# Kernel tuning notes

Measured on AMD Instinct MI355X. Metric: run time of the kernel, lower is better.

Reference implementation:

```python
import jax, jax.numpy as jnp
import numpy as np
from jax import lax

D = 1024
T = 1024
B = 8


def setup_inputs() -> dict:
    key = jax.random.key(0)
    ks = jax.random.split(key, 4)
    x = jax.random.normal(ks[0], (T, B, D), dtype=jnp.float32)
    h0 = jnp.zeros((B, D), dtype=jnp.float32)
    # xavier-ish scale for input projections, small orthogonal-like scale for W_h
    xav = float(np.sqrt(2.0 / (D + D)))
    W_alpha = jax.random.normal(ks[1], (D, D), dtype=jnp.float32) * xav
    b_alpha = jnp.full((D,), 2.0, dtype=jnp.float32)  # init_alpha_bias=2.0
    W_h = jax.random.normal(ks[2], (D, D), dtype=jnp.float32) * (0.5 / np.sqrt(D))
    W_x = jax.random.normal(ks[3], (D, D), dtype=jnp.float32) * xav
    b = jnp.zeros((D,), dtype=jnp.float32)
    return {"x": x, "h0": h0, "W_alpha": W_alpha, "b_alpha": b_alpha,
            "W_h": W_h, "W_x": W_x, "b": b}


def reference(x, h0, W_alpha, b_alpha, W_h, W_x, b):
    # x: [T,B,D], h0: [B,D]; E63a nonlinear delta recurrence.
    # Precompute input-dependent parts (parallel over T), scan the recurrence.
    alpha_all = jax.nn.sigmoid(jnp.einsum('tbd,ed->tbe', x, W_alpha) + b_alpha)  # [T,B,D]
    wx_all = jnp.einsum('tbd,ed->tbe', x, W_x) + b                               # [T,B,D]

    def step(h_prev, inp):
        alpha, wx = inp
        v = jnp.tanh(h_prev @ W_h.T + wx)          # nonlinear value in h
        h_new = alpha * h_prev + (1.0 - alpha) * v  # complementary gate
        out = h_new * jax.nn.silu(h_new)            # gated output
        return h_new, (h_new, out)

    _, (hs, outs) = lax.scan(step, h0, (alpha_all, wx_all))
    h = jnp.concatenate([h0[None], hs], axis=0)  # [T+1,B,D] (matches torch path)
    return outs, h
```

## Files before the change

kernel.cpp:

```cpp
#include <hip/hip_runtime.h>
#include <hip/hip_bf16.h>
#include <hip/hip_cooperative_groups.h>

typedef __attribute__((ext_vector_type(8))) short bf16x8;
typedef __attribute__((ext_vector_type(4))) float f32x4;
typedef __attribute__((ext_vector_type(4))) unsigned int u32x4;

#define D_ 1024
#define T_ 1024
#define B_ 8
#define M_ (T_ * B_)

__device__ __forceinline__ float ldv(const float* p) { return *p; }
__device__ __forceinline__ float ldv(const __hip_bfloat16* p) { return __bfloat162float(*p); }
__device__ __forceinline__ void stv(float* p, float v) { *p = v; }
__device__ __forceinline__ void stv(__hip_bfloat16* p, float v) { *p = __float2bfloat16(v); }

__device__ __forceinline__ u32x4 ld_chunk(const unsigned* p) {
  u32x4 v;
  asm volatile("global_load_dwordx4 %0, %1, off sc0 sc1" : "=v"(v) : "v"(p) : "memory");
  return v;
}
__device__ __forceinline__ void st_word(unsigned* p, unsigned v) {
  asm volatile("global_store_dword %0, %1, off sc0 sc1" :: "v"(p), "v"(v) : "memory");
}
__device__ __forceinline__ void wait_vm0() {
  asm volatile("s_waitcnt vmcnt(0)" ::: "memory");
}
__device__ __forceinline__ void bar_lds() {
  asm volatile("s_waitcnt lgkmcnt(0)\n\ts_barrier" ::: "memory");
  __builtin_amdgcn_sched_barrier(0);
}
__device__ __forceinline__ float exp2_fast(float x) {
  float r;
  asm("v_exp_f32 %0, %1" : "=v"(r) : "v"(x));
  return r;
}
__device__ __forceinline__ float rcp_fast(float x) {
  float r;
  asm("v_rcp_f32 %0, %1" : "=v"(r) : "v"(x));
  return r;
}

__global__ __launch_bounds__(256) void conv_bf16(const float* __restrict__ in,
                                                 __hip_bfloat16* __restrict__ out,
                                                 int n8)
{
  int i = blockIdx.x * blockDim.x + threadIdx.x;
  const int stride = gridDim.x * blockDim.x;
  for (; i < n8; i += stride) {
    const f32x4* p = reinterpret_cast<const f32x4*>(in + (size_t)i * 8);
    f32x4 a = p[0], b = p[1];
    union { bf16x8 v; __hip_bfloat16 e[8]; } u;
#pragma unroll
    for (int j = 0; j < 4; ++j) {
      u.e[j] = __float2bfloat16(a[j]);
      u.e[j + 4] = __float2bfloat16(b[j]);
    }
    *reinterpret_cast<bf16x8*>(out + (size_t)i * 8) = u.v;
  }
}

template <typename ST>
__global__ __launch_bounds__(256) void gemm_front(
    const __hip_bfloat16* __restrict__ xb,
    const __hip_bfloat16* __restrict__ Wab,
    const float* __restrict__ ba,
    const __hip_bfloat16* __restrict__ Wxb,
    const float* __restrict__ bbias,
    ST* __restrict__ alpha_out,
    ST* __restrict__ wx_out)
{
  const int tid = threadIdx.x;
  const int lane = tid & 63;
  const int w = tid >> 6;
  const int r = lane & 15;
  const int g = lane >> 4;
  const bool isA = blockIdx.y < 8;
  const int m0 = blockIdx.x * 128 + (w >> 1) * 64;
  const int n0 = (blockIdx.y & 7) * 128 + (w & 1) * 64;
  const __hip_bfloat16* __restrict__ W = isA ? Wab : Wxb;
  ST* __restrict__ outp = isA ? alpha_out : wx_out;

  f32x4 acc[4][4] = {};

  const __hip_bfloat16* aBase = xb + (size_t)(m0 + r) * D_ + g * 8;
  const __hip_bfloat16* bBase = W + (size_t)(n0 + r) * D_ + g * 8;

  for (int k = 0; k < D_; k += 32) {
    bf16x8 a[4], b[4];
#pragma unroll
    for (int mt = 0; mt < 4; ++mt)
      a[mt] = *reinterpret_cast<const bf16x8*>(aBase + (size_t)mt * 16 * D_ + k);
#pragma unroll
    for (int nt = 0; nt < 4; ++nt)
      b[nt] = *reinterpret_cast<const bf16x8*>(bBase + (size_t)nt * 16 * D_ + k);
#pragma unroll
    for (int mt = 0; mt < 4; ++mt)
#pragma unroll
      for (int nt = 0; nt < 4; ++nt)
        acc[mt][nt] = __builtin_amdgcn_mfma_f32_16x16x32_bf16(a[mt], b[nt], acc[mt][nt], 0, 0, 0);
  }

#pragma unroll
  for (int nt = 0; nt < 4; ++nt) {
    const int col = n0 + nt * 16 + r;
    const float bias = isA ? ba[col] : bbias[col];
#pragma unroll
    for (int mt = 0; mt < 4; ++mt) {
      const int row = m0 + mt * 16 + g * 4;
#pragma unroll
      for (int i = 0; i < 4; ++i) {
        float v = acc[mt][nt][i] + bias;
        if (isA) v = 1.0f / (1.0f + expf(-v));
        stv(outp + (size_t)(row + i) * D_ + col, v);
      }
    }
  }
}

template <typename ST>
__global__ __launch_bounds__(256) void scan_rec(
    const float* __restrict__ h0,
    const float* __restrict__ Wh,
    const ST* __restrict__ alpha_all,
    const ST* __restrict__ wx_all,
    unsigned* __restrict__ ring,
    float* __restrict__ out_outs,
    float* __restrict__ out_h)
{
  __shared__ __align__(16) unsigned short W_lds[64 * 1024];
  __shared__ __align__(16) unsigned short h_lds[1024];
  __shared__ float C_lds[4][64];

  const int tid = threadIdx.x;
  const int lane = tid & 63;
  const int w = tid >> 6;
  const int r = lane & 15;
  const int g = lane >> 4;
  const int bb = blockIdx.x & 7;
  const int s = blockIdx.x >> 3;
  const int e0 = s * 64;

  for (int idx = tid; idx < 64 * 128; idx += 256) {
    const int row = idx >> 7;
    const int k8 = (idx & 127) * 8;
    const f32x4* p = reinterpret_cast<const f32x4*>(Wh + (size_t)(e0 + row) * D_ + k8);
    f32x4 a = p[0], bv = p[1];
    union { bf16x8 v; __hip_bfloat16 e[8]; } u;
#pragma unroll
    for (int j = 0; j < 4; ++j) {
      u.e[j] = __float2bfloat16(a[j]);
      u.e[j + 4] = __float2bfloat16(bv[j]);
    }
    const unsigned byteoff = ((unsigned)row * 2048u + (unsigned)k8 * 2u) ^ (((unsigned)row & 7u) << 4);
    *reinterpret_cast<bf16x8*>(reinterpret_cast<char*>(W_lds) + byteoff) = u.v;
  }

  float h_f = 0.0f, wx_c = 0.0f, al_c = 0.0f;
  if (tid < 64) {
    const int e = e0 + tid;
    h_f = h0[bb * D_ + e];
    out_h[(size_t)bb * D_ + e] = h_f;
    const unsigned short hb = ((__hip_bfloat16_raw)__float2bfloat16(h_f)).x;
    h_lds[e] = hb;
    st_word(ring + (size_t)bb * 1024 + e, (unsigned)hb | (1u << 16));
    wx_c = ldv(wx_all + (size_t)bb * D_ + e);
    al_c = ldv(alpha_all + (size_t)bb * D_ + e);
  }
  __syncthreads();

  for (int t = 0; t < T_; ++t) {
    const unsigned want = (unsigned)(t + 1);
    const int kk = w * 256 + lane * 8;
    if (lane < 32 && (kk >> 6) != s) {
      const unsigned* cp = ring + ((size_t)(t & 1) * B_ + bb) * 1024 + kk;
      u32x4 A, Bv;
      int bail = 0;
      for (;;) {
        A = ld_chunk(cp);
        Bv = ld_chunk(cp + 4);
        wait_vm0();
        const bool ok = (A[0] >> 16) == want && (A[1] >> 16) == want &&
                        (A[2] >> 16) == want && (A[3] >> 16) == want &&
                        (Bv[0] >> 16) == want && (Bv[1] >> 16) == want &&
                        (Bv[2] >> 16) == want && (Bv[3] >> 16) == want;
        if (__all(ok)) break;
        if (++bail > (1 << 20)) break;
      }
      u32x4 hw;
      hw[0] = (A[0] & 0xffffu) | (A[1] << 16);
      hw[1] = (A[2] & 0xffffu) | (A[3] << 16);
      hw[2] = (Bv[0] & 0xffffu) | (Bv[1] << 16);
      hw[3] = (Bv[2] & 0xffffu) | (Bv[3] << 16);
      *reinterpret_cast<u32x4*>(&h_lds[kk]) = hw;
    }
    asm volatile("s_waitcnt lgkmcnt(0)" ::: "memory");
    __builtin_amdgcn_sched_barrier(0);

    f32x4 acc[4] = {};
#pragma unroll
    for (int kt = 0; kt < 8; ++kt) {
      const int k = w * 256 + kt * 32 + g * 8;
      bf16x8 afrag = {};
      if (r == 0)
        afrag = *reinterpret_cast<const bf16x8*>(&h_lds[k]);
#pragma unroll
      for (int nt = 0; nt < 4; ++nt) {
        const unsigned row = (unsigned)(nt * 16 + r);
        const unsigned byteoff = (row * 2048u + (unsigned)k * 2u) ^ ((row & 7u) << 4);
        bf16x8 bfrag = *reinterpret_cast<const bf16x8*>(
            reinterpret_cast<const char*>(W_lds) + byteoff);
        acc[nt] = __builtin_amdgcn_mfma_f32_16x16x32_bf16(afrag, bfrag, acc[nt], 0, 0, 0);
      }
    }
    if (g == 0) {
#pragma unroll
      for (int nt = 0; nt < 4; ++nt)
        C_lds[w][nt * 16 + r] = acc[nt][0];
    }
    bar_lds();

    if (tid < 64) {
      const int e = e0 + tid;
      const float y = C_lds[0][tid] + C_lds[1][tid] + C_lds[2][tid] + C_lds[3][tid];
      const float xs = (y + wx_c) * 2.8853900817779268f;
      const float tv = fmaf(-2.0f, rcp_fast(exp2_fast(xs) + 1.0f), 1.0f);
      h_f = fmaf(al_c, h_f - tv, tv);
      const unsigned short hb = ((__hip_bfloat16_raw)__float2bfloat16(h_f)).x;
      h_lds[e] = hb;
      st_word(ring + ((size_t)((t + 1) & 1) * B_ + bb) * 1024 + e,
              (unsigned)hb | ((unsigned)(t + 2) << 16));
      const float sg = rcp_fast(1.0f + exp2_fast(h_f * -1.4426950408889634f));
      const float o = h_f * h_f * sg;
      out_h[(size_t)(t + 1) * (B_ * D_) + (size_t)bb * D_ + e] = h_f;
      out_outs[(size_t)t * (B_ * D_) + (size_t)bb * D_ + e] = o;
      if (t + 1 < T_) {
        wx_c = ldv(wx_all + (size_t)((t + 1) * B_ + bb) * D_ + e);
        al_c = ldv(alpha_all + (size_t)((t + 1) * B_ + bb) * D_ + e);
      }
    }
    bar_lds();
  }
}

template <typename ST>
static void launch_all(const float* x, const float* h0, const float* Wa,
                       const float* ba, const float* Wh, const float* Wx,
                       const float* bb, __hip_bfloat16* xb, __hip_bfloat16* Wab,
                       __hip_bfloat16* Wxb, ST* alpha_buf, ST* wx_buf,
                       unsigned* ring, float* out_outs, float* out_h,
                       hipStream_t stream)
{
  const size_t ringBytes = (size_t)2 * B_ * 1024 * 4;
  hipMemsetAsync(ring, 0, ringBytes, stream);
  conv_bf16<<<dim3(2048), dim3(256), 0, stream>>>(x, xb, M_ * D_ / 8);
  conv_bf16<<<dim3(512), dim3(256), 0, stream>>>(Wa, Wab, D_ * D_ / 8);
  conv_bf16<<<dim3(512), dim3(256), 0, stream>>>(Wx, Wxb, D_ * D_ / 8);
  gemm_front<ST><<<dim3(64, 16), dim3(256), 0, stream>>>(xb, Wab, ba, Wxb, bb,
                                                         alpha_buf, wx_buf);
  void* args[] = {(void*)&h0,     (void*)&Wh,   (void*)&alpha_buf,
                  (void*)&wx_buf, (void*)&ring, (void*)&out_outs,
                  (void*)&out_h};
  hipLaunchCooperativeKernel(reinterpret_cast<void*>(&scan_rec<ST>), dim3(128),
                             dim3(256), args, 0, stream);
}

extern "C" void kernel_launch(void* const* d_in, const int* in_sizes, int n_in,
                              void* d_out, int out_size, void* d_ws,
                              size_t ws_size, hipStream_t stream)
{
  const float* x = (const float*)d_in[0];
  const float* h0 = (const float*)d_in[1];
  const float* Wa = (const float*)d_in[2];
  const float* ba = (const float*)d_in[3];
  const float* Wh = (const float*)d_in[4];
  const float* Wx = (const float*)d_in[5];
  const float* bb = (const float*)d_in[6];

  float* out_outs = (float*)d_out;
  float* out_h = out_outs + (size_t)T_ * B_ * D_;

  char* ws = (char*)d_ws;
  const size_t nMD = (size_t)M_ * D_;
  const size_t nDD = (size_t)D_ * D_;

  __hip_bfloat16* xb = (__hip_bfloat16*)ws;
  __hip_bfloat16* Wab = (__hip_bfloat16*)(ws + nMD * 2);
  __hip_bfloat16* Wxb = (__hip_bfloat16*)(ws + nMD * 2 + nDD * 2);
  char* rest = ws + nMD * 2 + 2 * nDD * 2;

  const size_t ringBytes = (size_t)2 * B_ * 1024 * 4;
  const size_t needF32 = (size_t)(rest - ws) + 2 * nMD * 4 + ringBytes;

  if (ws_size >= needF32) {
    float* alpha_buf = (float*)rest;
    float* wx_buf = (float*)(rest + nMD * 4);
    unsigned* ring = (unsigned*)(rest + 2 * nMD * 4);
    launch_all<float>(x, h0, Wa, ba, Wh, Wx, bb, xb, Wab, Wxb, alpha_buf,
                      wx_buf, ring, out_outs, out_h, stream);
  } else {
    __hip_bfloat16* alpha_buf = (__hip_bfloat16*)rest;
    __hip_bfloat16* wx_buf = (__hip_bfloat16*)(rest + nMD * 2);
    unsigned* ring = (unsigned*)(rest + 2 * nMD * 2);
    launch_all<__hip_bfloat16>(x, h0, Wa, ba, Wh, Wx, bb, xb, Wab, Wxb,
                               alpha_buf, wx_buf, ring, out_outs, out_h,
                               stream);
  }
}
```

Measured before the change: 1.764 ms.

## Stage front GEMM tiles through double-buffered LDS with register prefetch

```diff
diff --git a/kernel.cpp b/kernel.cpp
--- a/kernel.cpp
+++ b/kernel.cpp
@@ -71,44 +71,87 @@
     ST* __restrict__ alpha_out,
     ST* __restrict__ wx_out)
 {
+  __shared__ __align__(16) unsigned short As[2][128 * 64];
+  __shared__ __align__(16) unsigned short Bs[2][128 * 64];
+
   const int tid = threadIdx.x;
   const int lane = tid & 63;
   const int w = tid >> 6;
   const int r = lane & 15;
   const int g = lane >> 4;
   const bool isA = blockIdx.y < 8;
-  const int m0 = blockIdx.x * 128 + (w >> 1) * 64;
-  const int n0 = (blockIdx.y & 7) * 128 + (w & 1) * 64;
+  const int m0 = blockIdx.x * 128;
+  const int n0 = (blockIdx.y & 7) * 128;
   const __hip_bfloat16* __restrict__ W = isA ? Wab : Wxb;
   ST* __restrict__ outp = isA ? alpha_out : wx_out;
 
+  const int sr = tid >> 1;
+  const int sc = (tid & 1) * 32;
+  const __hip_bfloat16* aSrc = xb + (size_t)(m0 + sr) * D_ + sc;
+  const __hip_bfloat16* bSrc = W + (size_t)(n0 + sr) * D_ + sc;
+
+  {
+#pragma unroll
+    for (int j = 0; j < 4; ++j) {
+      bf16x8 av = *reinterpret_cast<const bf16x8*>(aSrc + j * 8);
+      bf16x8 bv = *reinterpret_cast<const bf16x8*>(bSrc + j * 8);
+      *reinterpret_cast<bf16x8*>(&As[0][sr * 64 + sc + j * 8]) = av;
+      *reinterpret_cast<bf16x8*>(&Bs[0][sr * 64 + sc + j * 8]) = bv;
+    }
+  }
+  __syncthreads();
+
   f32x4 acc[4][4] = {};
-
-  const __hip_bfloat16* aBase = xb + (size_t)(m0 + r) * D_ + g * 8;
-  const __hip_bfloat16* bBase = W + (size_t)(n0 + r) * D_ + g * 8;
-
-  for (int k = 0; k < D_; k += 32) {
-    bf16x8 a[4], b[4];
-#pragma unroll
-    for (int mt = 0; mt < 4; ++mt)
-      a[mt] = *reinterpret_cast<const bf16x8*>(aBase + (size_t)mt * 16 * D_ + k);
-#pragma unroll
-    for (int nt = 0; nt < 4; ++nt)
-      b[nt] = *reinterpret_cast<const bf16x8*>(bBase + (size_t)nt * 16 * D_ + k);
-#pragma unroll
-    for (int mt = 0; mt < 4; ++mt)
+  const int wrow = (w >> 1) * 64;
+  const int wcol = (w & 1) * 64;
+
+  for (int kt = 0; kt < 16; ++kt) {
+    const int cur = kt & 1;
+    const bool more = (kt + 1 < 16);
+    bf16x8 anx[4], bnx[4];
+    if (more) {
+      const int kn = (kt + 1) * 64;
+#pragma unroll
+      for (int j = 0; j < 4; ++j) {
+        anx[j] = *reinterpret_cast<const bf16x8*>(aSrc + kn + j * 8);
+        bnx[j] = *reinterpret_cast<const bf16x8*>(bSrc + kn + j * 8);
+      }
+    }
+#pragma unroll
+    for (int ks = 0; ks < 2; ++ks) {
+      bf16x8 af[4], bf[4];
+#pragma unroll
+      for (int mt = 0; mt < 4; ++mt)
+        af[mt] = *reinterpret_cast<const bf16x8*>(
+            &As[cur][(wrow + mt * 16 + r) * 64 + ks * 32 + g * 8]);
 #pragma unroll
       for (int nt = 0; nt < 4; ++nt)
-        acc[mt][nt] = __builtin_amdgcn_mfma_f32_16x16x32_bf16(a[mt], b[nt], acc[mt][nt], 0, 0, 0);
+        bf[nt] = *reinterpret_cast<const bf16x8*>(
+            &Bs[cur][(wcol + nt * 16 + r) * 64 + ks * 32 + g * 8]);
+#pragma unroll
+      for (int mt = 0; mt < 4; ++mt)
+#pragma unroll
+        for (int nt = 0; nt < 4; ++nt)
+          acc[mt][nt] = __builtin_amdgcn_mfma_f32_16x16x32_bf16(
+              af[mt], bf[nt], acc[mt][nt], 0, 0, 0);
+    }
+    if (more) {
+#pragma unroll
+      for (int j = 0; j < 4; ++j) {
+        *reinterpret_cast<bf16x8*>(&As[cur ^ 1][sr * 64 + sc + j * 8]) = anx[j];
+        *reinterpret_cast<bf16x8*>(&Bs[cur ^ 1][sr * 64 + sc + j * 8]) = bnx[j];
+      }
+    }
+    __syncthreads();
   }
 
 #pragma unroll
   for (int nt = 0; nt < 4; ++nt) {
-    const int col = n0 + nt * 16 + r;
+    const int col = n0 + wcol + nt * 16 + r;
     const float bias = isA ? ba[col] : bbias[col];
 #pragma unroll
     for (int mt = 0; mt < 4; ++mt) {
-      const int row = m0 + mt * 16 + g * 4;
+      const int row = m0 + wrow + mt * 16 + g * 4;
 #pragma unroll
       for (int i = 0; i < 4; ++i) {
         float v = acc[mt][nt][i] + bias;
```

Result: faster. 1.690 ms (-4.2%).
